# Kernel optimization log

Measured on AMD Instinct MI355X. Metric: run time of the kernel, lower is better.

Reference implementation:

```python
import jax, jax.numpy as jnp
import numpy as np

N = 30000        # num nodes
R = 16           # num relations
B = 30           # num bases (hard-coded in source)
E = 960000       # num edges (avg degree 32)
IN, HID, OUT, ADR = 128, 128, 64, 400


def setup_inputs() -> dict:
    key = jax.random.key(0)
    ks = jax.random.split(key, 13)
    s_in = 1.0 / np.sqrt(IN)
    s_hid = 1.0 / np.sqrt(HID)
    s_out = 1.0 / np.sqrt(OUT)
    return {
        "x": jax.random.normal(ks[0], (N, IN), jnp.float32),
        "edge_index": jax.random.randint(ks[1], (2, E), 0, N, jnp.int64),
        "edge_type": jax.random.randint(ks[2], (E,), 0, R, jnp.int64),
        "comp1": jax.random.normal(ks[3], (R, B), jnp.float32) * (1.0 / np.sqrt(B)),
        "basis1": jax.random.normal(ks[4], (B, IN, HID), jnp.float32) * s_in,
        "root1": jax.random.normal(ks[5], (IN, HID), jnp.float32) * s_in,
        "bias1": jnp.zeros((HID,), jnp.float32),
        "comp2": jax.random.normal(ks[6], (R, B), jnp.float32) * (1.0 / np.sqrt(B)),
        "basis2": jax.random.normal(ks[7], (B, HID, OUT), jnp.float32) * s_hid,
        "root2": jax.random.normal(ks[8], (HID, OUT), jnp.float32) * s_hid,
        "bias2": jnp.zeros((OUT,), jnp.float32),
        "wc": jax.random.normal(ks[9], (OUT, ADR), jnp.float32) * s_out,
        "bc": jnp.zeros((ADR,), jnp.float32),
    }


def _rgcn_conv(x, src, dst, etype, comp, basis, root, bias):
    """PyG RGCNConv: out[i] = sum_r mean_{e: dst=i, rel=r} x[src_e] @ W_r + x[i] @ root + bias,
    with basis decomposition W_r = sum_b comp[r,b] * basis[b].
    Aggregate-first: segment-mean x[src] into (node, relation) buckets, then contract."""
    n, din = x.shape
    seg = dst * R + etype                                   # [E] composite segment id
    msg = x[src]                                            # [E, din] edge gather
    sums = jax.ops.segment_sum(msg, seg, num_segments=n * R)            # [N*R, din]
    cnt = jax.ops.segment_sum(jnp.ones((src.shape[0],), x.dtype), seg,
                              num_segments=n * R)                       # [N*R]
    mean = sums / jnp.maximum(cnt, 1.0)[:, None]            # per-relation mean
    agg = mean.reshape(n, R, din)                           # [N, R, din]
    w = jnp.einsum('rb,bio->rio', comp, basis)              # [R, din, dout]
    return jnp.einsum('nri,rio->no', agg, w) + x @ root + bias


def reference(x, edge_index, edge_type, comp1, basis1, root1, bias1,
              comp2, basis2, root2, bias2, wc, bc):
    src, dst = edge_index[0], edge_index[1]
    h = _rgcn_conv(x, src, dst, edge_type, comp1, basis1, root1, bias1)
    h = jax.nn.relu(h)
    h = _rgcn_conv(h, src, dst, edge_type, comp2, basis2, root2, bias2)
    return h @ wc + bc
```

## Files before the change

kernel.cpp:

```cpp
#include <hip/hip_runtime.h>

#define R_    16
#define NBAS  30
#define DIN1  128
#define DHID  128
#define DOUT2 64
#define DADR  400
#define KCH   128
#define LDB   ((R_ + 1) * 128)

typedef __attribute__((ext_vector_type(8))) short bf16x8;
typedef __attribute__((ext_vector_type(4))) float f32x4;

__device__ __forceinline__ short f2bf(float f) {
    unsigned u = __float_as_uint(f);
    u += 0x7fffu + ((u >> 16) & 1u);
    return (short)(u >> 16);
}
__device__ __forceinline__ unsigned packbf(float lo, float hi) {
    return (unsigned)(unsigned short)f2bf(lo) | ((unsigned)(unsigned short)f2bf(hi) << 16);
}

struct Row8 { f32x4 lo, hi; };

__device__ __forceinline__ Row8 row8_zero() {
    Row8 z; z.lo = (f32x4){0.f,0.f,0.f,0.f}; z.hi = (f32x4){0.f,0.f,0.f,0.f}; return z;
}
__device__ __forceinline__ Row8 row8_add(Row8 a, int4 v) {
    unsigned u0 = (unsigned)v.x, u1 = (unsigned)v.y, u2 = (unsigned)v.z, u3 = (unsigned)v.w;
    a.lo[0] += __uint_as_float(u0 << 16);
    a.lo[1] += __uint_as_float(u0 & 0xffff0000u);
    a.lo[2] += __uint_as_float(u1 << 16);
    a.lo[3] += __uint_as_float(u1 & 0xffff0000u);
    a.hi[0] += __uint_as_float(u2 << 16);
    a.hi[1] += __uint_as_float(u2 & 0xffff0000u);
    a.hi[2] += __uint_as_float(u3 << 16);
    a.hi[3] += __uint_as_float(u3 & 0xffff0000u);
    return a;
}
__device__ __forceinline__ int4 row8_pack(Row8 a) {
    int4 o;
    o.x = (int)packbf(a.lo[0], a.lo[1]);
    o.y = (int)packbf(a.lo[2], a.lo[3]);
    o.z = (int)packbf(a.hi[0], a.hi[1]);
    o.w = (int)packbf(a.hi[2], a.hi[3]);
    return o;
}

__device__ __forceinline__ Row8 make_arow(const short* __restrict__ featbf,
                                          const int* __restrict__ off2,
                                          const int* __restrict__ srt,
                                          int r, int grow, int N, int l16) {
    Row8 a = row8_zero();
    if (grow >= N) return a;
    if (r < R_) {
        int seg = r * N + grow;
        int beg = off2[seg], end = off2[seg + 1];
        int p = beg;
        for (; p + 2 <= end; p += 2) {
            int s0 = srt[p], s1 = srt[p + 1];
            int4 v0 = *(const int4*)(featbf + (size_t)s0 * KCH + l16 * 8);
            int4 v1 = *(const int4*)(featbf + (size_t)s1 * KCH + l16 * 8);
            a = row8_add(a, v0);
            a = row8_add(a, v1);
        }
        if (p < end) {
            int4 v0 = *(const int4*)(featbf + (size_t)srt[p] * KCH + l16 * 8);
            a = row8_add(a, v0);
        }
        int c = end - beg;
        float sc = 1.f / (float)(c > 1 ? c : 1);
        a.lo *= sc; a.hi *= sc;
    } else {
        int4 v = *(const int4*)(featbf + (size_t)grow * KCH + l16 * 8);
        a = row8_add(a, v);
    }
    return a;
}

__global__ __launch_bounds__(256) void tobf_kernel(const float* __restrict__ in,
                                                   short* __restrict__ out, int n4) {
    int i = blockIdx.x * 256 + threadIdx.x;
    if (i >= n4) return;
    float4 v = ((const float4*)in)[i];
    short4 b = { f2bf(v.x), f2bf(v.y), f2bf(v.z), f2bf(v.w) };
    ((short4*)out)[i] = b;
}

__global__ __launch_bounds__(256) void count_kernel(const int* __restrict__ dst,
                                                    const int* __restrict__ ety,
                                                    int* __restrict__ cnt, int E, int N) {
    int e = blockIdx.x * blockDim.x + threadIdx.x;
    if (e < E) atomicAdd(&cnt[ety[e] * N + dst[e]], 1);
}

#define SCAN_CHUNK 2048
#define SCAN_IT    8

__global__ __launch_bounds__(256) void scan_bsum_kernel(const int* __restrict__ cnt, int nseg,
                                                        int* __restrict__ bsum) {
    __shared__ int sd[256];
    int base = blockIdx.x * SCAN_CHUNK;
    int s = 0;
    #pragma unroll
    for (int j = 0; j < SCAN_IT; ++j) {
        int idx = base + j * 256 + threadIdx.x;
        if (idx < nseg) s += cnt[idx];
    }
    sd[threadIdx.x] = s;
    __syncthreads();
    for (int st = 128; st > 0; st >>= 1) {
        if (threadIdx.x < st) sd[threadIdx.x] += sd[threadIdx.x + st];
        __syncthreads();
    }
    if (threadIdx.x == 0) bsum[blockIdx.x] = sd[0];
}

__global__ __launch_bounds__(256) void scan_top_kernel(const int* __restrict__ bsum, int nblk,
                                                       int* __restrict__ boff,
                                                       int* __restrict__ off, int nseg) {
    if (nblk > 256) {
        if (threadIdx.x == 0) {
            int run = 0;
            for (int i = 0; i < nblk; ++i) { int t = bsum[i]; boff[i] = run; run += t; }
            off[nseg] = run;
        }
        return;
    }
    __shared__ int sd[256];
    int v = (threadIdx.x < nblk) ? bsum[threadIdx.x] : 0;
    sd[threadIdx.x] = v;
    __syncthreads();
    for (int st = 1; st < 256; st <<= 1) {
        int t = (threadIdx.x >= st) ? sd[threadIdx.x - st] : 0;
        __syncthreads();
        sd[threadIdx.x] += t;
        __syncthreads();
    }
    if (threadIdx.x < nblk) boff[threadIdx.x] = sd[threadIdx.x] - v;
    if (threadIdx.x == nblk - 1) off[nseg] = sd[threadIdx.x];
}

__global__ __launch_bounds__(256) void scan_final_kernel(const int* __restrict__ cnt, int nseg,
                                                         const int* __restrict__ boff,
                                                         int* __restrict__ off,
                                                         int* __restrict__ cursor) {
    __shared__ int sd[256];
    int base = blockIdx.x * SCAN_CHUNK + threadIdx.x * SCAN_IT;
    int v[SCAN_IT];
    int s = 0;
    #pragma unroll
    for (int j = 0; j < SCAN_IT; ++j) {
        int idx = base + j;
        v[j] = (idx < nseg) ? cnt[idx] : 0;
        s += v[j];
    }
    sd[threadIdx.x] = s;
    __syncthreads();
    for (int st = 1; st < 256; st <<= 1) {
        int t = (threadIdx.x >= st) ? sd[threadIdx.x - st] : 0;
        __syncthreads();
        sd[threadIdx.x] += t;
        __syncthreads();
    }
    int run = boff[blockIdx.x] + sd[threadIdx.x] - s;
    #pragma unroll
    for (int j = 0; j < SCAN_IT; ++j) {
        int idx = base + j;
        if (idx < nseg) { off[idx] = run; cursor[idx] = run; }
        run += v[j];
    }
}

__global__ __launch_bounds__(256) void reorder_kernel(const int* __restrict__ src,
                                                      const int* __restrict__ dst,
                                                      const int* __restrict__ ety,
                                                      int* __restrict__ cursor,
                                                      int* __restrict__ srt, int E, int N) {
    int e = blockIdx.x * blockDim.x + threadIdx.x;
    if (e >= E) return;
    int seg = ety[e] * N + dst[e];
    int pos = atomicAdd(&cursor[seg], 1);
    srt[pos] = src[e];
}

#define PREP1 (R_ * DIN1 * DHID)
#define PREP2 (PREP1 + R_ * DHID * DOUT2)
#define PREP3 (PREP2 + DIN1 * DHID)
#define PREP4 (PREP3 + DHID * DOUT2)
#define PREP5 (PREP4 + DADR * DOUT2)
__global__ __launch_bounds__(256) void prep_kernel(const float* __restrict__ comp1,
                                                   const float* __restrict__ basis1,
                                                   const float* __restrict__ root1,
                                                   const float* __restrict__ comp2,
                                                   const float* __restrict__ basis2,
                                                   const float* __restrict__ root2,
                                                   const float* __restrict__ wc,
                                                   short* __restrict__ BT1,
                                                   short* __restrict__ BT2,
                                                   short* __restrict__ wcT) {
    int idx = blockIdx.x * 256 + threadIdx.x;
    if (idx < PREP1) {
        int o = idx % DHID, i = (idx / DHID) % DIN1, r = idx / (DHID * DIN1);
        float acc = 0.f;
        #pragma unroll 6
        for (int b = 0; b < NBAS; ++b)
            acc += comp1[r * NBAS + b] * basis1[((size_t)b * DIN1 + i) * DHID + o];
        BT1[(size_t)o * LDB + r * DIN1 + i] = f2bf(acc);
    } else if (idx < PREP2) {
        int t = idx - PREP1;
        int o = t % DOUT2, i = (t / DOUT2) % DHID, r = t / (DOUT2 * DHID);
        float acc = 0.f;
        #pragma unroll 6
        for (int b = 0; b < NBAS; ++b)
            acc += comp2[r * NBAS + b] * basis2[((size_t)b * DHID + i) * DOUT2 + o];
        BT2[(size_t)o * LDB + r * DHID + i] = f2bf(acc);
    } else if (idx < PREP3) {
        int t = idx - PREP2;
        int o = t % DHID, i = t / DHID;
        BT1[(size_t)o * LDB + R_ * DIN1 + i] = f2bf(root1[(size_t)i * DHID + o]);
    } else if (idx < PREP4) {
        int t = idx - PREP3;
        int o = t % DOUT2, i = t / DOUT2;
        BT2[(size_t)o * LDB + R_ * DHID + i] = f2bf(root2[(size_t)i * DOUT2 + o]);
    } else if (idx < PREP5) {
        int t = idx - PREP4;
        int a = t / DOUT2, k = t % DOUT2;
        wcT[(size_t)a * DOUT2 + k] = f2bf(wc[(size_t)k * DADR + a]);
    }
}

template<int BN, bool OUTBF>
__global__ __launch_bounds__(256)
void rgcn_fused_kernel(const short* __restrict__ featbf,
                       const int* __restrict__ off2,
                       const int* __restrict__ srt,
                       const short* __restrict__ BT,
                       const float* __restrict__ bias,
                       void* __restrict__ Hout, int N, int relu)
{
    constexpr int BM = 32, BK = 128;
    constexpr int WN = BN / 4;
    constexpr int MR = 2;
    constexpr int NR = WN / 16;
    constexpr int BL = BN / 16;

    __shared__ short lA[BM * BK];
    __shared__ short lB[BN * BK];

    const int tid  = threadIdx.x;
    const int lane = tid & 63;
    const int wv   = tid >> 6;
    const int g16  = tid >> 4;
    const int l16  = tid & 15;
    const int n0   = blockIdx.x * BM;
    const int row0 = n0 + g16;
    const int row1 = n0 + 16 + g16;

    f32x4 acc[MR][NR];
    #pragma unroll
    for (int m = 0; m < MR; ++m)
        #pragma unroll
        for (int n = 0; n < NR; ++n)
            acc[m][n] = (f32x4){0.f, 0.f, 0.f, 0.f};

    for (int r = 0; r <= R_; ++r) {
        if (r) __syncthreads();

        #pragma unroll
        for (int j = 0; j < BL; ++j) {
            int o = j * 16 + g16;
            int4 v = *(const int4*)(BT + (size_t)o * LDB + r * BK + l16 * 8);
            int byte = ((o * BK + l16 * 8) << 1) ^ ((o & 15) << 4);
            *(int4*)((char*)lB + byte) = v;
        }

        {
            Row8 a = make_arow(featbf, off2, srt, r, row0, N, l16);
            int byte = ((g16 * BK + l16 * 8) << 1) ^ ((g16 & 15) << 4);
            *(int4*)((char*)lA + byte) = row8_pack(a);
        }
        {
            Row8 a = make_arow(featbf, off2, srt, r, row1, N, l16);
            int rowl = 16 + g16;
            int byte = ((rowl * BK + l16 * 8) << 1) ^ ((rowl & 15) << 4);
            *(int4*)((char*)lA + byte) = row8_pack(a);
        }
        __syncthreads();

        #pragma unroll
        for (int kk = 0; kk < BK / 32; ++kk) {
            const int kpos = kk * 32 + (lane >> 4) * 8;
            bf16x8 af[MR], bfr[NR];
            #pragma unroll
            for (int m = 0; m < MR; ++m) {
                int row = m * 16 + (lane & 15);
                af[m] = *(const bf16x8*)((const char*)lA +
                         (((row * BK + kpos) << 1) ^ ((row & 15) << 4)));
            }
            #pragma unroll
            for (int n = 0; n < NR; ++n) {
                int col = wv * WN + n * 16 + (lane & 15);
                bfr[n] = *(const bf16x8*)((const char*)lB +
                         (((col * BK + kpos) << 1) ^ ((col & 15) << 4)));
            }
            #pragma unroll
            for (int m = 0; m < MR; ++m)
                #pragma unroll
                for (int n = 0; n < NR; ++n)
                    acc[m][n] = __builtin_amdgcn_mfma_f32_16x16x32_bf16(
                        af[m], bfr[n], acc[m][n], 0, 0, 0);
        }
    }

    #pragma unroll
    for (int m = 0; m < MR; ++m)
        #pragma unroll
        for (int n = 0; n < NR; ++n)
            #pragma unroll
            for (int i = 0; i < 4; ++i) {
                int row  = m * 16 + ((lane >> 4) << 2) + i;
                int col  = wv * WN + n * 16 + (lane & 15);
                int grow = n0 + row;
                if (grow >= N) continue;
                float v = acc[m][n][i] + bias[col];
                if (relu) v = fmaxf(v, 0.f);
                if (OUTBF) ((short*)Hout)[(size_t)grow * BN + col] = f2bf(v);
                else       ((float*)Hout)[(size_t)grow * BN + col] = v;
            }
}

__global__ __launch_bounds__(256)
void classifier_gemm_kernel(const short* __restrict__ h2bf,
                            const short* __restrict__ wcT,
                            const float* __restrict__ bc,
                            float* __restrict__ out, int N)
{
    constexpr int BM = 128, BN = 80, BK = 64;
    constexpr int MR = 2, NR = 5;

    __shared__ short lA[BM * BK];
    __shared__ short lB[BN * BK];

    const int tid  = threadIdx.x;
    const int lane = tid & 63;
    const int wv   = tid >> 6;
    const int nodeBase = blockIdx.x * BM;
    const int colBase  = blockIdx.y * BN;

    const int t8  = tid & 7;
    const int r32 = tid >> 3;

    #pragma unroll
    for (int it = 0; it < 4; ++it) {
        int row  = it * 32 + r32;
        int grow = nodeBase + row;
        int4 v = {0, 0, 0, 0};
        if (grow < N) v = *(const int4*)(h2bf + (size_t)grow * DOUT2 + t8 * 8);
        int byte = ((row * BK + t8 * 8) << 1) ^ ((row & 7) << 4);
        *(int4*)((char*)lA + byte) = v;
    }
    for (int o = r32; o < BN; o += 32) {
        int4 v = *(const int4*)(wcT + (size_t)(colBase + o) * DOUT2 + t8 * 8);
        int byte = ((o * BK + t8 * 8) << 1) ^ ((o & 7) << 4);
        *(int4*)((char*)lB + byte) = v;
    }
    __syncthreads();

    f32x4 acc[MR][NR];
    #pragma unroll
    for (int m = 0; m < MR; ++m)
        #pragma unroll
        for (int n = 0; n < NR; ++n)
            acc[m][n] = (f32x4){0.f, 0.f, 0.f, 0.f};

    #pragma unroll
    for (int kk = 0; kk < BK / 32; ++kk) {
        const int kpos = kk * 32 + (lane >> 4) * 8;
        bf16x8 af[MR], bfr[NR];
        #pragma unroll
        for (int m = 0; m < MR; ++m) {
            int row = wv * 32 + m * 16 + (lane & 15);
            af[m] = *(const bf16x8*)((const char*)lA +
                     (((row * BK + kpos) << 1) ^ ((row & 7) << 4)));
        }
        #pragma unroll
        for (int n = 0; n < NR; ++n) {
            int col = n * 16 + (lane & 15);
            bfr[n] = *(const bf16x8*)((const char*)lB +
                     (((col * BK + kpos) << 1) ^ ((col & 7) << 4)));
        }
        #pragma unroll
        for (int m = 0; m < MR; ++m)
            #pragma unroll
            for (int n = 0; n < NR; ++n)
                acc[m][n] = __builtin_amdgcn_mfma_f32_16x16x32_bf16(
                    af[m], bfr[n], acc[m][n], 0, 0, 0);
    }

    #pragma unroll
    for (int m = 0; m < MR; ++m)
        #pragma unroll
        for (int n = 0; n < NR; ++n)
            #pragma unroll
            for (int i = 0; i < 4; ++i) {
                int row  = wv * 32 + m * 16 + ((lane >> 4) << 2) + i;
                int col  = n * 16 + (lane & 15);
                int grow = nodeBase + row;
                if (grow >= N) continue;
                int gcol = colBase + col;
                out[(size_t)grow * DADR + gcol] = acc[m][n][i] + bc[gcol];
            }
}

static inline size_t align16(size_t x) { return (x + 15) & ~(size_t)15; }

extern "C" void kernel_launch(void* const* d_in, const int* in_sizes, int n_in,
                              void* d_out, int out_size, void* d_ws, size_t ws_size,
                              hipStream_t stream) {
    const float* x      = (const float*)d_in[0];
    const int*   ei     = (const int*)d_in[1];
    const int*   et     = (const int*)d_in[2];
    const float* comp1  = (const float*)d_in[3];
    const float* basis1 = (const float*)d_in[4];
    const float* root1  = (const float*)d_in[5];
    const float* bias1  = (const float*)d_in[6];
    const float* comp2  = (const float*)d_in[7];
    const float* basis2 = (const float*)d_in[8];
    const float* root2  = (const float*)d_in[9];
    const float* bias2  = (const float*)d_in[10];
    const float* wc     = (const float*)d_in[11];
    const float* bc     = (const float*)d_in[12];
    float* out = (float*)d_out;

    const int E = in_sizes[1] / 2;
    const int N = in_sizes[0] / DIN1;
    const int* srcp = ei;
    const int* dstp = ei + E;

    const int NSEG = N * R_;
    const int NBLK = (NSEG + SCAN_CHUNK - 1) / SCAN_CHUNK;

    char* ws = (char*)d_ws;
    size_t o = 0;
    int*   cntI   = (int*)(ws + o);   o = align16(o + (size_t)NSEG * 4);
    int*   off2   = (int*)(ws + o);   o = align16(o + (size_t)(NSEG + 1) * 4);
    int*   cursor = (int*)(ws + o);   o = align16(o + (size_t)NSEG * 4);
    int*   bsum   = (int*)(ws + o);   o = align16(o + (size_t)NBLK * 4);
    int*   boff   = (int*)(ws + o);   o = align16(o + (size_t)NBLK * 4);
    int*   srt    = (int*)(ws + o);   o = align16(o + (size_t)E * 4);
    short* BT1    = (short*)(ws + o); o = align16(o + (size_t)DHID * LDB * 2);
    short* BT2    = (short*)(ws + o); o = align16(o + (size_t)DOUT2 * LDB * 2);
    short* wcTb   = (short*)(ws + o); o = align16(o + (size_t)DADR * DOUT2 * 2);
    short* xbf    = (short*)(ws + o); o = align16(o + (size_t)N * DIN1 * 2);
    short* h1bf   = (short*)(ws + o); o = align16(o + (size_t)N * DHID * 2);
    short* h2bf   = (short*)(ws + o); o = align16(o + (size_t)N * DOUT2 * 2);

    const int n4 = N * DIN1 / 4;
    tobf_kernel<<<(n4 + 255) / 256, 256, 0, stream>>>(x, xbf, n4);

    hipMemsetAsync(cntI, 0, (size_t)NSEG * 4, stream);
    count_kernel<<<(E + 255) / 256, 256, 0, stream>>>(dstp, et, cntI, E, N);
    scan_bsum_kernel<<<NBLK, 256, 0, stream>>>(cntI, NSEG, bsum);
    scan_top_kernel<<<1, 256, 0, stream>>>(bsum, NBLK, boff, off2, NSEG);
    scan_final_kernel<<<NBLK, 256, 0, stream>>>(cntI, NSEG, boff, off2, cursor);
    reorder_kernel<<<(E + 255) / 256, 256, 0, stream>>>(srcp, dstp, et, cursor, srt, E, N);

    prep_kernel<<<(PREP5 + 255) / 256, 256, 0, stream>>>(comp1, basis1, root1,
                                                         comp2, basis2, root2, wc,
                                                         BT1, BT2, wcTb);

    const int gGrid = (N + 31) / 32;
    rgcn_fused_kernel<DHID, true><<<gGrid, 256, 0, stream>>>(xbf,  off2, srt, BT1, bias1, h1bf, N, 1);
    rgcn_fused_kernel<DOUT2, true><<<gGrid, 256, 0, stream>>>(h1bf, off2, srt, BT2, bias2, h2bf, N, 0);

    dim3 cGrid((N + 127) / 128, DADR / 80);
    classifier_gemm_kernel<<<cGrid, 256, 0, stream>>>(h2bf, wcTb, bc, out, N);
}
```

Baseline: 352.8 us.

## Double-buffer gathered rows, read weights directly, shrink row tile, shuffle edge indices

The fused RGCN kernel now processes 16 nodes per block instead of 32. The A tile is double-buffered so the gather for relation r+1 overlaps the MFMAs for relation r, with one barrier per relation. Weight B fragments are read straight from global/L2 instead of staged in LDS, and up to 16 neighbour indices are loaded once per row and broadcast with shuffles. This adds more blocks and an occupancy hint. The trade-off is extra global weight traffic per block and halved MFMA reuse of each B fragment.

```diff
diff --git a/kernel.cpp b/kernel.cpp
--- a/kernel.cpp
+++ b/kernel.cpp
@@ -47,33 +47,37 @@
     return o;
 }
 
-__device__ __forceinline__ Row8 make_arow(const short* __restrict__ featbf,
-                                          const int* __restrict__ off2,
-                                          const int* __restrict__ srt,
-                                          int r, int grow, int N, int l16) {
+__device__ __forceinline__ Row8 gather_row(const short* __restrict__ featbf,
+                                           const int* __restrict__ off2,
+                                           const int* __restrict__ srt,
+                                           int r, int row, int N, int l16) {
     Row8 a = row8_zero();
-    if (grow >= N) return a;
+    if (row >= N) return a;
     if (r < R_) {
-        int seg = r * N + grow;
-        int beg = off2[seg], end = off2[seg + 1];
-        int p = beg;
-        for (; p + 2 <= end; p += 2) {
-            int s0 = srt[p], s1 = srt[p + 1];
-            int4 v0 = *(const int4*)(featbf + (size_t)s0 * KCH + l16 * 8);
-            int4 v1 = *(const int4*)(featbf + (size_t)s1 * KCH + l16 * 8);
+        int seg = r * N + row;
+        int b = off2[seg];
+        int c = off2[seg + 1] - b;
+        int s = c < 16 ? c : 16;
+        int idx = (l16 < s) ? srt[b + l16] : 0;
+        int j = 0;
+        for (; j + 2 <= s; j += 2) {
+            int i0 = __shfl(idx, j, 16);
+            int i1 = __shfl(idx, j + 1, 16);
+            int4 v0 = *(const int4*)(featbf + (size_t)i0 * KCH + l16 * 8);
+            int4 v1 = *(const int4*)(featbf + (size_t)i1 * KCH + l16 * 8);
             a = row8_add(a, v0);
             a = row8_add(a, v1);
         }
-        if (p < end) {
-            int4 v0 = *(const int4*)(featbf + (size_t)srt[p] * KCH + l16 * 8);
-            a = row8_add(a, v0);
-        }
-        int c = end - beg;
+        if (j < s) {
+            int i0 = __shfl(idx, j, 16);
+            a = row8_add(a, *(const int4*)(featbf + (size_t)i0 * KCH + l16 * 8));
+        }
+        for (int p = b + 16; p < b + c; ++p)
+            a = row8_add(a, *(const int4*)(featbf + (size_t)srt[p] * KCH + l16 * 8));
         float sc = 1.f / (float)(c > 1 ? c : 1);
         a.lo *= sc; a.hi *= sc;
     } else {
-        int4 v = *(const int4*)(featbf + (size_t)grow * KCH + l16 * 8);
-        a = row8_add(a, v);
+        a = row8_add(a, *(const int4*)(featbf + (size_t)row * KCH + l16 * 8));
     }
     return a;
 }
@@ -231,7 +235,7 @@
 }
 
 template<int BN, bool OUTBF>
-__global__ __launch_bounds__(256)
+__global__ __launch_bounds__(256, 6)
 void rgcn_fused_kernel(const short* __restrict__ featbf,
                        const int* __restrict__ off2,
                        const int* __restrict__ srt,
@@ -239,14 +243,11 @@
                        const float* __restrict__ bias,
                        void* __restrict__ Hout, int N, int relu)
 {
-    constexpr int BM = 32, BK = 128;
+    constexpr int BM = 16, BK = 128;
     constexpr int WN = BN / 4;
-    constexpr int MR = 2;
     constexpr int NR = WN / 16;
-    constexpr int BL = BN / 16;
-
-    __shared__ short lA[BM * BK];
-    __shared__ short lB[BN * BK];
+
+    __shared__ short lA[2][BM * BK];
 
     const int tid  = threadIdx.x;
     const int lane = tid & 63;
@@ -254,80 +255,59 @@
     const int g16  = tid >> 4;
     const int l16  = tid & 15;
     const int n0   = blockIdx.x * BM;
-    const int row0 = n0 + g16;
-    const int row1 = n0 + 16 + g16;
-
-    f32x4 acc[MR][NR];
-    #pragma unroll
-    for (int m = 0; m < MR; ++m)
-        #pragma unroll
-        for (int n = 0; n < NR; ++n)
-            acc[m][n] = (f32x4){0.f, 0.f, 0.f, 0.f};
+    const int row  = n0 + g16;
+
+    f32x4 acc[NR];
+    #pragma unroll
+    for (int n = 0; n < NR; ++n)
+        acc[n] = (f32x4){0.f, 0.f, 0.f, 0.f};
+
+    const int abyte = ((g16 * BK + l16 * 8) << 1) ^ ((g16 & 15) << 4);
+
+    {
+        Row8 a = gather_row(featbf, off2, srt, 0, row, N, l16);
+        *(int4*)((char*)lA[0] + abyte) = row8_pack(a);
+    }
+    __syncthreads();
 
     for (int r = 0; r <= R_; ++r) {
-        if (r) __syncthreads();
-
-        #pragma unroll
-        for (int j = 0; j < BL; ++j) {
-            int o = j * 16 + g16;
-            int4 v = *(const int4*)(BT + (size_t)o * LDB + r * BK + l16 * 8);
-            int byte = ((o * BK + l16 * 8) << 1) ^ ((o & 15) << 4);
-            *(int4*)((char*)lB + byte) = v;
-        }
-
-        {
-            Row8 a = make_arow(featbf, off2, srt, r, row0, N, l16);
-            int byte = ((g16 * BK + l16 * 8) << 1) ^ ((g16 & 15) << 4);
-            *(int4*)((char*)lA + byte) = row8_pack(a);
-        }
-        {
-            Row8 a = make_arow(featbf, off2, srt, r, row1, N, l16);
-            int rowl = 16 + g16;
-            int byte = ((rowl * BK + l16 * 8) << 1) ^ ((rowl & 15) << 4);
-            *(int4*)((char*)lA + byte) = row8_pack(a);
-        }
-        __syncthreads();
+        const char* lAc = (const char*)lA[r & 1];
+
+        Row8 an = row8_zero();
+        if (r < R_) an = gather_row(featbf, off2, srt, r + 1, row, N, l16);
 
         #pragma unroll
         for (int kk = 0; kk < BK / 32; ++kk) {
-            const int kpos = kk * 32 + (lane >> 4) * 8;
-            bf16x8 af[MR], bfr[NR];
-            #pragma unroll
-            for (int m = 0; m < MR; ++m) {
-                int row = m * 16 + (lane & 15);
-                af[m] = *(const bf16x8*)((const char*)lA +
-                         (((row * BK + kpos) << 1) ^ ((row & 15) << 4)));
-            }
+            const int kpos = kk * 32 + ((lane >> 4) << 3);
+            const int arow = lane & 15;
+            bf16x8 af = *(const bf16x8*)(lAc +
+                         (((arow * BK + kpos) << 1) ^ ((arow & 15) << 4)));
             #pragma unroll
             for (int n = 0; n < NR; ++n) {
                 int col = wv * WN + n * 16 + (lane & 15);
-                bfr[n] = *(const bf16x8*)((const char*)lB +
-                         (((col * BK + kpos) << 1) ^ ((col & 15) << 4)));
+                bf16x8 bfr = *(const bf16x8*)(BT + (size_t)col * LDB + r * BK + kpos);
+                acc[n] = __builtin_amdgcn_mfma_f32_16x16x32_bf16(af, bfr, acc[n], 0, 0, 0);
             }
-            #pragma unroll
-            for (int m = 0; m < MR; ++m)
-                #pragma unroll
-                for (int n = 0; n < NR; ++n)
-                    acc[m][n] = __builtin_amdgcn_mfma_f32_16x16x32_bf16(
-                        af[m], bfr[n], acc[m][n], 0, 0, 0);
-        }
-    }
-
-    #pragma unroll
-    for (int m = 0; m < MR; ++m)
-        #pragma unroll
-        for (int n = 0; n < NR; ++n)
-            #pragma unroll
-            for (int i = 0; i < 4; ++i) {
-                int row  = m * 16 + ((lane >> 4) << 2) + i;
-                int col  = wv * WN + n * 16 + (lane & 15);
-                int grow = n0 + row;
-                if (grow >= N) continue;
-                float v = acc[m][n][i] + bias[col];
-                if (relu) v = fmaxf(v, 0.f);
-                if (OUTBF) ((short*)Hout)[(size_t)grow * BN + col] = f2bf(v);
-                else       ((float*)Hout)[(size_t)grow * BN + col] = v;
-            }
+        }
+
+        if (r < R_)
+            *(int4*)((char*)lA[(r + 1) & 1] + abyte) = row8_pack(an);
+        __syncthreads();
+    }
+
+    #pragma unroll
+    for (int n = 0; n < NR; ++n)
+        #pragma unroll
+        for (int i = 0; i < 4; ++i) {
+            int rrow = ((lane >> 4) << 2) + i;
+            int col  = wv * WN + n * 16 + (lane & 15);
+            int grow = n0 + rrow;
+            if (grow >= N) continue;
+            float v = acc[n][i] + bias[col];
+            if (relu) v = fmaxf(v, 0.f);
+            if (OUTBF) ((short*)Hout)[(size_t)grow * BN + col] = f2bf(v);
+            else       ((float*)Hout)[(size_t)grow * BN + col] = v;
+        }
 }
 
 __global__ __launch_bounds__(256)
@@ -470,7 +450,7 @@
                                                          comp2, basis2, root2, wc,
                                                          BT1, BT2, wcTb);
 
-    const int gGrid = (N + 31) / 32;
+    const int gGrid = (N + 15) / 16;
     rgcn_fused_kernel<DHID, true><<<gGrid, 256, 0, stream>>>(xbf,  off2, srt, BT1, bias1, h1bf, N, 1);
     rgcn_fused_kernel<DOUT2, true><<<gGrid, 256, 0, stream>>>(h1bf, off2, srt, BT2, bias2, h2bf, N, 0);
 
```

Measured after the change: 392.3 us. +11.2%, slower.
